# Optimization experiments

Measured on AMD Instinct MI355X. Metric: run time of the kernel, lower is better.

Reference implementation:

```python
import jax, jax.numpy as jnp
import numpy as np

N = 10000       # nodes
E = 640000      # edges (avg degree 64)
F_IN = 128      # num_node_features
H = 128         # hid_size
C = 16          # num_classes


def setup_inputs() -> dict:
    key = jax.random.key(0)
    ks = jax.random.split(key, 12)
    g = lambda k, shape, fan: jax.random.normal(k, shape, jnp.float32) * (1.0 / np.sqrt(fan))
    return {
        "x": jax.random.normal(ks[0], (N, F_IN), jnp.float32),
        "edge_index": jax.random.randint(ks[1], (2, E), 0, N, dtype=jnp.int32),
        "W1": g(ks[2], (F_IN, H), F_IN), "b1": jnp.zeros((H,), jnp.float32),
        "W2": g(ks[3], (H, H), H),       "b2": jnp.zeros((H,), jnp.float32),
        "Wlin1": g(ks[4], (H, C), H),    "blin1": jnp.zeros((C,), jnp.float32),
        "Wdeg2": g(ks[5], (H, 1), H),    "bdeg2": jnp.zeros((1,), jnp.float32),
        "Wdeg3": g(ks[6], (H, 1), H),    "bdeg3": jnp.zeros((1,), jnp.float32),
        "Wdown": g(ks[7], (F_IN, H), F_IN), "bdown": jnp.zeros((H,), jnp.float32),
    }


def _gcn_norm(edge_index):
    # PyG GCNConv: add self-loops, symmetric normalization d^-1/2 A d^-1/2
    loops = jnp.arange(N, dtype=edge_index.dtype)
    src = jnp.concatenate([edge_index[0], loops])   # [E+N]
    dst = jnp.concatenate([edge_index[1], loops])   # [E+N]
    deg = jax.ops.segment_sum(jnp.ones_like(dst, jnp.float32), dst, num_segments=N)
    dis = jnp.where(deg > 0, jax.lax.rsqrt(jnp.maximum(deg, 1.0)), 0.0)
    norm = dis[src] * dis[dst]                      # [E+N]
    return src, dst, norm


def _gcn_conv(h, W, b, src, dst, norm):
    h = h @ W                                       # [N, H] transform first (smaller dim)
    msg = h[src] * norm[:, None]                    # gather + edge weight
    return jax.ops.segment_sum(msg, dst, num_segments=N) + b


def reference(x, edge_index, W1, b1, W2, b2, Wlin1, blin1, Wdeg2, bdeg2, Wdeg3, bdeg3, Wdown, bdown):
    src, dst, norm = _gcn_norm(edge_index)
    original = x @ Wdown + bdown                    # down_sample residual
    h = jax.nn.relu(_gcn_conv(x, W1, b1, src, dst, norm))
    # dropout is identity in eval mode
    h = _gcn_conv(h, W2, b2, src, dst, norm) + original
    result1 = jax.nn.log_softmax(h @ Wlin1 + blin1, axis=1)   # [N, C]
    result2 = (h @ Wdeg2 + bdeg2)[:, 0]                        # [N]
    result3 = (h @ Wdeg3 + bdeg3)[:, 0]                        # [N]
    return (result1, result2, result3)
```

## Files before the change

### kernel.cpp

```cpp
#include <hip/hip_runtime.h>
#include <math.h>

#define N_NODES 10000
#define N_EDGES 640000
#define NB      100
#define CH      (N_EDGES / NB)
#define HP      10016

typedef unsigned short ushort4_t __attribute__((ext_vector_type(4)));
typedef unsigned short ushort8_t __attribute__((ext_vector_type(8)));

__device__ inline unsigned short f2bf(float f) {
    unsigned int u = __float_as_uint(f);
    u = (u + 0x7FFFu + ((u >> 16) & 1u)) >> 16;
    return (unsigned short)u;
}
__device__ inline float bf2f(unsigned short s) {
    return __uint_as_float(((unsigned int)s) << 16);
}

__global__ __launch_bounds__(256) void k_hist(const int* __restrict__ dst,
                                              int* __restrict__ h) {
    __shared__ int hs[HP];
    int t = threadIdx.x;
    for (int j = t; j < HP; j += 256) hs[j] = 0;
    __syncthreads();
    int base = blockIdx.x * CH;
#pragma unroll 4
    for (int j = t; j < CH; j += 256) atomicAdd(&hs[dst[base + j]], 1);
    __syncthreads();
    int* out = h + blockIdx.x * HP;
    for (int j = t; j < N_NODES; j += 256) out[j] = hs[j];
}

__global__ __launch_bounds__(256) void k_colsum(const int* __restrict__ h,
                                                int* __restrict__ deg,
                                                float* __restrict__ dis) {
    int i = blockIdx.x * blockDim.x + threadIdx.x;
    if (i >= N_NODES) return;
    int s = 0;
#pragma unroll 10
    for (int b = 0; b < NB; ++b) s += h[b * HP + i];
    deg[i] = s;
    dis[i] = rsqrtf((float)(s + 1));
}

__global__ void k_scan(const int* __restrict__ deg, int* __restrict__ offsets, int n) {
    __shared__ int sums[1024];
    int tid = threadIdx.x;
    const int per = (n + 1023) / 1024;
    int start = tid * per;
    int end   = min(start + per, n);
    int s = 0;
    for (int i = start; i < end; ++i) s += deg[i];
    sums[tid] = s;
    __syncthreads();
    for (int off = 1; off < 1024; off <<= 1) {
        int t = (tid >= off) ? sums[tid - off] : 0;
        __syncthreads();
        sums[tid] += t;
        __syncthreads();
    }
    int run = sums[tid] - s;
    for (int i = start; i < end; ++i) {
        offsets[i] = run;
        run += deg[i];
    }
    if (tid == 1023) offsets[n] = sums[1023];
}

__global__ __launch_bounds__(256) void k_base(const int* __restrict__ h,
                                              const int* __restrict__ offsets,
                                              int* __restrict__ base) {
    int i = blockIdx.x * blockDim.x + threadIdx.x;
    if (i >= N_NODES) return;
    int run = offsets[i];
#pragma unroll 10
    for (int b = 0; b < NB; ++b) {
        base[b * HP + i] = run;
        run += h[b * HP + i];
    }
}

__global__ __launch_bounds__(256) void k_scatter(const int* __restrict__ src,
                                                 const int* __restrict__ dst,
                                                 const int* __restrict__ base,
                                                 int* __restrict__ csr) {
    __shared__ int cur[N_NODES];
    int t = threadIdx.x;
    const int* mybase = base + blockIdx.x * HP;
    for (int j = t; j < N_NODES; j += 256) cur[j] = mybase[j];
    __syncthreads();
    int off = blockIdx.x * CH;
#pragma unroll 4
    for (int j = t; j < CH; j += 256) {
        int d = dst[off + j];
        int s = src[off + j];
        int p = atomicAdd(&cur[d], 1);
        csr[p] = s;
    }
}

template <int BF16OUT>
__global__ __launch_bounds__(256) void k_gemm(const float* __restrict__ X,
                                              const float* __restrict__ W,
                                              const float* __restrict__ bias,
                                              void* __restrict__ Yv, int n) {
    __shared__ float xs[32 * 128];
    __shared__ float ws[128 * 128];
    int t = threadIdx.x;
    int tile0 = blockIdx.x * 32;

    const float4* Wv = (const float4*)W;
    float4* wsv = (float4*)ws;
#pragma unroll
    for (int q = 0; q < 16; ++q) wsv[t + 256 * q] = Wv[t + 256 * q];

    const float4* Xv = (const float4*)X;
    float4* xsv = (float4*)xs;
#pragma unroll
    for (int q = 0; q < 4; ++q) {
        int idx = t + 256 * q;
        int row = tile0 + (idx >> 5);
        float4 v = make_float4(0.f, 0.f, 0.f, 0.f);
        if (row < n) v = Xv[(size_t)row * 32 + (idx & 31)];
        xsv[idx] = v;
    }
    __syncthreads();

    int c4 = t & 31;
    int rg = t >> 5;
    float4 acc[4];
#pragma unroll
    for (int p = 0; p < 4; ++p) acc[p] = make_float4(0.f, 0.f, 0.f, 0.f);

    const float4* wsr = (const float4*)ws;
    const float4* xsr = (const float4*)xs;
#pragma unroll 4
    for (int kq = 0; kq < 32; ++kq) {
        float4 w0 = wsr[(4 * kq + 0) * 32 + c4];
        float4 w1 = wsr[(4 * kq + 1) * 32 + c4];
        float4 w2 = wsr[(4 * kq + 2) * 32 + c4];
        float4 w3 = wsr[(4 * kq + 3) * 32 + c4];
#pragma unroll
        for (int p = 0; p < 4; ++p) {
            float4 xv = xsr[(rg * 4 + p) * 32 + kq];
            acc[p].x += xv.x * w0.x + xv.y * w1.x + xv.z * w2.x + xv.w * w3.x;
            acc[p].y += xv.x * w0.y + xv.y * w1.y + xv.z * w2.y + xv.w * w3.y;
            acc[p].z += xv.x * w0.z + xv.y * w1.z + xv.z * w2.z + xv.w * w3.z;
            acc[p].w += xv.x * w0.w + xv.y * w1.w + xv.z * w2.w + xv.w * w3.w;
        }
    }
    float4 bv = make_float4(0.f, 0.f, 0.f, 0.f);
    if (bias) bv = ((const float4*)bias)[c4];
#pragma unroll
    for (int p = 0; p < 4; ++p) {
        int row = tile0 + rg * 4 + p;
        if (row < n) {
            float ox = acc[p].x + bv.x, oy = acc[p].y + bv.y;
            float oz = acc[p].z + bv.z, ow = acc[p].w + bv.w;
            if (BF16OUT) {
                ushort4_t o;
                o[0] = f2bf(ox); o[1] = f2bf(oy); o[2] = f2bf(oz); o[3] = f2bf(ow);
                ((ushort4_t*)Yv)[(size_t)row * 32 + c4] = o;
            } else {
                ((float4*)Yv)[(size_t)row * 32 + c4] = make_float4(ox, oy, oz, ow);
            }
        }
    }
}

template <int MODE>
__global__ __launch_bounds__(256) void k_agg(const unsigned short* __restrict__ T,
                                             const float* __restrict__ dis,
                                             const int* __restrict__ offsets,
                                             const int* __restrict__ csr,
                                             const float* __restrict__ bias,
                                             const float* __restrict__ resid,
                                             float* __restrict__ Y, int n) {
    __shared__ float red[3][16][9];
    int i = blockIdx.x;
    int t = threadIdx.x;
    int c8 = t & 15;
    int es = t >> 4;
    int wave = t >> 6;
    int lane = t & 63;

    int e0 = offsets[i], e1 = offsets[i + 1];
    const ushort8_t* T8 = (const ushort8_t*)T;

    float acc[8];
#pragma unroll
    for (int j = 0; j < 8; ++j) acc[j] = 0.f;

    int e = e0 + es;
    for (; e + 16 < e1; e += 32) {
        int s0 = csr[e];
        int s1 = csr[e + 16];
        float w0 = dis[s0];
        float w1 = dis[s1];
        ushort8_t v0 = T8[(size_t)s0 * 16 + c8];
        ushort8_t v1 = T8[(size_t)s1 * 16 + c8];
#pragma unroll
        for (int j = 0; j < 8; ++j)
            acc[j] += w0 * bf2f(v0[j]) + w1 * bf2f(v1[j]);
    }
    if (e < e1) {
        int s0 = csr[e];
        float w0 = dis[s0];
        ushort8_t v0 = T8[(size_t)s0 * 16 + c8];
#pragma unroll
        for (int j = 0; j < 8; ++j) acc[j] += w0 * bf2f(v0[j]);
    }

#pragma unroll
    for (int j = 0; j < 8; ++j) {
        acc[j] += __shfl_xor(acc[j], 16, 64);
        acc[j] += __shfl_xor(acc[j], 32, 64);
    }
    if (wave > 0 && lane < 16) {
#pragma unroll
        for (int j = 0; j < 8; ++j) red[wave - 1][lane][j] = acc[j];
    }
    __syncthreads();
    if (wave == 0 && lane < 16) {
#pragma unroll
        for (int j = 0; j < 8; ++j)
            acc[j] += red[0][lane][j] + red[1][lane][j] + red[2][lane][j];

        float di = dis[i];
        ushort8_t sv = T8[(size_t)i * 16 + c8];
#pragma unroll
        for (int j = 0; j < 8; ++j) acc[j] += di * bf2f(sv[j]);

#pragma unroll
        for (int j = 0; j < 8; ++j) acc[j] = di * acc[j] + bias[c8 * 8 + j];

        if (MODE == 1) {
#pragma unroll
            for (int j = 0; j < 8; ++j) acc[j] = fmaxf(acc[j], 0.f);
        } else {
            const float4* rv4 = (const float4*)resid;
            float4 r0 = rv4[(size_t)i * 32 + c8 * 2];
            float4 r1 = rv4[(size_t)i * 32 + c8 * 2 + 1];
            acc[0] += r0.x; acc[1] += r0.y; acc[2] += r0.z; acc[3] += r0.w;
            acc[4] += r1.x; acc[5] += r1.y; acc[6] += r1.z; acc[7] += r1.w;
        }
        float4* Y4 = (float4*)Y;
        Y4[(size_t)i * 32 + c8 * 2]     = make_float4(acc[0], acc[1], acc[2], acc[3]);
        Y4[(size_t)i * 32 + c8 * 2 + 1] = make_float4(acc[4], acc[5], acc[6], acc[7]);
    }
}

__global__ __launch_bounds__(256) void k_heads(const float* __restrict__ h,
                                               const float* __restrict__ Wlin,
                                               const float* __restrict__ blin,
                                               const float* __restrict__ Wd2,
                                               const float* __restrict__ bd2,
                                               const float* __restrict__ Wd3,
                                               const float* __restrict__ bd3,
                                               float* __restrict__ out1,
                                               float* __restrict__ out2,
                                               float* __restrict__ out3, int n) {
    int wid = (blockIdx.x * blockDim.x + threadIdx.x) >> 6;
    int lane = threadIdx.x & 63;
    if (wid >= n) return;
    int r = wid;
    float h0 = h[(size_t)r * 128 + lane];
    float h1 = h[(size_t)r * 128 + 64 + lane];
    float p2 = h0 * Wd2[lane] + h1 * Wd2[64 + lane];
    float p3 = h0 * Wd3[lane] + h1 * Wd3[64 + lane];
#pragma unroll
    for (int d = 1; d < 64; d <<= 1) {
        p2 += __shfl_xor(p2, d, 64);
        p3 += __shfl_xor(p3, d, 64);
    }
    if (lane == 0) {
        out2[r] = p2 + bd2[0];
        out3[r] = p3 + bd3[0];
    }
    int c = lane & 15, kg = lane >> 4;
    float z = 0.f;
#pragma unroll 8
    for (int j = 0; j < 32; ++j) {
        int k = kg * 32 + j;
        z += h[(size_t)r * 128 + k] * Wlin[k * 16 + c];
    }
    z += __shfl_xor(z, 16, 64);
    z += __shfl_xor(z, 32, 64);
    z += blin[c];
    float m = z;
#pragma unroll
    for (int d = 1; d < 16; d <<= 1) m = fmaxf(m, __shfl_xor(m, d, 64));
    float ex = expf(z - m);
    float ssum = ex;
#pragma unroll
    for (int d = 1; d < 16; d <<= 1) ssum += __shfl_xor(ssum, d, 64);
    float lsm = z - m - logf(ssum);
    if (lane < 16) out1[(size_t)r * 16 + c] = lsm;
}

extern "C" void kernel_launch(void* const* d_in, const int* in_sizes, int n_in,
                              void* d_out, int out_size, void* d_ws, size_t ws_size,
                              hipStream_t stream) {
    const float* x     = (const float*)d_in[0];
    const int*   ei    = (const int*)d_in[1];
    const float* W1    = (const float*)d_in[2];
    const float* b1    = (const float*)d_in[3];
    const float* W2    = (const float*)d_in[4];
    const float* b2    = (const float*)d_in[5];
    const float* Wlin1 = (const float*)d_in[6];
    const float* blin1 = (const float*)d_in[7];
    const float* Wdeg2 = (const float*)d_in[8];
    const float* bdeg2 = (const float*)d_in[9];
    const float* Wdeg3 = (const float*)d_in[10];
    const float* bdeg3 = (const float*)d_in[11];
    const float* Wdown = (const float*)d_in[12];
    const float* bdown = (const float*)d_in[13];

    const int n = N_NODES, E = N_EDGES;
    const int* src = ei;
    const int* dst = ei + E;

    char* ws = (char*)d_ws;
    int*            hmat    = (int*)ws;
    int*            bmat    = hmat + NB * HP;
    int*            deg     = bmat + NB * HP;
    int*            offsets = deg + HP;
    float*          dis     = (float*)(offsets + HP);
    int*            csr     = (int*)(dis + HP);
    unsigned short* bufT    = (unsigned short*)(csr + E);
    float*          bufB    = (float*)(bufT + (size_t)n * 128);
    float*          bufC    = bufB + (size_t)n * 128;

    k_hist<<<NB, 256, 0, stream>>>(dst, hmat);
    k_colsum<<<(n + 255) / 256, 256, 0, stream>>>(hmat, deg, dis);
    k_scan<<<1, 1024, 0, stream>>>(deg, offsets, n);
    k_base<<<(n + 255) / 256, 256, 0, stream>>>(hmat, offsets, bmat);
    k_scatter<<<NB, 256, 0, stream>>>(src, dst, bmat, csr);

    k_gemm<1><<<(n + 31) / 32, 256, 0, stream>>>(x, W1, nullptr, bufT, n);
    k_gemm<0><<<(n + 31) / 32, 256, 0, stream>>>(x, Wdown, bdown, bufB, n);
    k_agg<1><<<n, 256, 0, stream>>>(bufT, dis, offsets, csr, b1, nullptr, bufC, n);
    k_gemm<1><<<(n + 31) / 32, 256, 0, stream>>>(bufC, W2, nullptr, bufT, n);
    k_agg<2><<<n, 256, 0, stream>>>(bufT, dis, offsets, csr, b2, bufB, bufC, n);

    float* out1 = (float*)d_out;
    float* out2 = out1 + (size_t)n * 16;
    float* out3 = out2 + n;
    k_heads<<<(n + 3) / 4, 256, 0, stream>>>(bufC, Wlin1, blin1, Wdeg2, bdeg2,
                                             Wdeg3, bdeg3, out1, out2, out3, n);
}
```

Baseline: 129.2 us.

## Fuse CSR build into one persistent kernel with grid barriers, merge gemms and heads

```diff
diff --git a/kernel.cpp b/kernel.cpp
--- a/kernel.cpp
+++ b/kernel.cpp
@@ -3,8 +3,9 @@
 
 #define N_NODES 10000
 #define N_EDGES 640000
-#define NB      100
-#define CH      (N_EDGES / NB)
+#define NBP     125
+#define CHP     (N_EDGES / NBP)
+#define NPB     (N_NODES / NBP)
 #define HP      10016
 
 typedef unsigned short ushort4_t __attribute__((ext_vector_type(4)));
@@ -19,97 +20,112 @@
     return __uint_as_float(((unsigned int)s) << 16);
 }
 
-__global__ __launch_bounds__(256) void k_hist(const int* __restrict__ dst,
-                                              int* __restrict__ h) {
+__device__ __forceinline__ void gbar(int* bar, int slot) {
+    __syncthreads();
+    if (threadIdx.x == 0) {
+        int* cnt = bar + slot;
+        int* gen = bar + 8 + slot;
+        int g = atomicAdd(gen, 0);
+        __threadfence();
+        if (atomicAdd(cnt, 1) == NBP - 1) {
+            __threadfence();
+            atomicAdd(gen, 1);
+        } else {
+            while (atomicAdd(gen, 0) == g) __builtin_amdgcn_s_sleep(4);
+        }
+        __threadfence();
+    }
+    __syncthreads();
+}
+
+__global__ __launch_bounds__(256) void k_prep(const int* __restrict__ src,
+                                              const int* __restrict__ dst,
+                                              int* bar,
+                                              int* __restrict__ hmat,
+                                              int* __restrict__ bmat,
+                                              int* __restrict__ rangesum,
+                                              int* __restrict__ offsets,
+                                              float* __restrict__ dis,
+                                              int* __restrict__ csr) {
     __shared__ int hs[HP];
-    int t = threadIdx.x;
+    __shared__ int ldeg[NPB];
+    __shared__ int lscan[NPB];
+    __shared__ int rs[NBP];
+    __shared__ int sP;
+    int b = blockIdx.x, t = threadIdx.x;
+
     for (int j = t; j < HP; j += 256) hs[j] = 0;
     __syncthreads();
-    int base = blockIdx.x * CH;
+    const int* mydst = dst + b * CHP;
 #pragma unroll 4
-    for (int j = t; j < CH; j += 256) atomicAdd(&hs[dst[base + j]], 1);
-    __syncthreads();
-    int* out = h + blockIdx.x * HP;
-    for (int j = t; j < N_NODES; j += 256) out[j] = hs[j];
-}
-
-__global__ __launch_bounds__(256) void k_colsum(const int* __restrict__ h,
-                                                int* __restrict__ deg,
-                                                float* __restrict__ dis) {
-    int i = blockIdx.x * blockDim.x + threadIdx.x;
-    if (i >= N_NODES) return;
-    int s = 0;
-#pragma unroll 10
-    for (int b = 0; b < NB; ++b) s += h[b * HP + i];
-    deg[i] = s;
-    dis[i] = rsqrtf((float)(s + 1));
-}
-
-__global__ void k_scan(const int* __restrict__ deg, int* __restrict__ offsets, int n) {
-    __shared__ int sums[1024];
-    int tid = threadIdx.x;
-    const int per = (n + 1023) / 1024;
-    int start = tid * per;
-    int end   = min(start + per, n);
-    int s = 0;
-    for (int i = start; i < end; ++i) s += deg[i];
-    sums[tid] = s;
-    __syncthreads();
-    for (int off = 1; off < 1024; off <<= 1) {
-        int t = (tid >= off) ? sums[tid - off] : 0;
-        __syncthreads();
-        sums[tid] += t;
-        __syncthreads();
-    }
-    int run = sums[tid] - s;
-    for (int i = start; i < end; ++i) {
+    for (int j = t; j < CHP; j += 256) atomicAdd(&hs[mydst[j]], 1);
+    __syncthreads();
+    int* hrow = hmat + b * HP;
+    for (int j = t; j < N_NODES; j += 256) hrow[j] = hs[j];
+    gbar(bar, 0);
+
+    int i0 = b * NPB;
+    if (t < NPB) {
+        int i = i0 + t;
+        int s = 0;
+#pragma unroll 5
+        for (int bb = 0; bb < NBP; ++bb) s += hmat[bb * HP + i];
+        ldeg[t] = s;
+        dis[i] = rsqrtf((float)(s + 1));
+    }
+    __syncthreads();
+    if (t == 0) {
+        int s = 0;
+        for (int j = 0; j < NPB; ++j) { lscan[j] = s; s += ldeg[j]; }
+        rangesum[b] = s;
+    }
+    gbar(bar, 1);
+
+    if (t < NBP) rs[t] = rangesum[t];
+    __syncthreads();
+    if (t == 0) {
+        int P = 0;
+        for (int bb = 0; bb < b; ++bb) P += rs[bb];
+        sP = P;
+        if (b == NBP - 1) offsets[N_NODES] = P + rs[b];
+    }
+    __syncthreads();
+    if (t < NPB) {
+        int i = i0 + t;
+        int run = sP + lscan[t];
         offsets[i] = run;
-        run += deg[i];
-    }
-    if (tid == 1023) offsets[n] = sums[1023];
-}
-
-__global__ __launch_bounds__(256) void k_base(const int* __restrict__ h,
-                                              const int* __restrict__ offsets,
-                                              int* __restrict__ base) {
-    int i = blockIdx.x * blockDim.x + threadIdx.x;
-    if (i >= N_NODES) return;
-    int run = offsets[i];
-#pragma unroll 10
-    for (int b = 0; b < NB; ++b) {
-        base[b * HP + i] = run;
-        run += h[b * HP + i];
-    }
-}
-
-__global__ __launch_bounds__(256) void k_scatter(const int* __restrict__ src,
-                                                 const int* __restrict__ dst,
-                                                 const int* __restrict__ base,
-                                                 int* __restrict__ csr) {
-    __shared__ int cur[N_NODES];
-    int t = threadIdx.x;
-    const int* mybase = base + blockIdx.x * HP;
-    for (int j = t; j < N_NODES; j += 256) cur[j] = mybase[j];
-    __syncthreads();
-    int off = blockIdx.x * CH;
+#pragma unroll 5
+        for (int bb = 0; bb < NBP; ++bb) {
+            bmat[bb * HP + i] = run;
+            run += hmat[bb * HP + i];
+        }
+    }
+    gbar(bar, 2);
+
+    const int* myb = bmat + b * HP;
+    for (int j = t; j < N_NODES; j += 256) hs[j] = myb[j];
+    __syncthreads();
+    const int* mysrc = src + b * CHP;
 #pragma unroll 4
-    for (int j = t; j < CH; j += 256) {
-        int d = dst[off + j];
-        int s = src[off + j];
-        int p = atomicAdd(&cur[d], 1);
+    for (int j = t; j < CHP; j += 256) {
+        int d = mydst[j];
+        int s = mysrc[j];
+        int p = atomicAdd(&hs[d], 1);
         csr[p] = s;
     }
 }
 
-template <int BF16OUT>
-__global__ __launch_bounds__(256) void k_gemm(const float* __restrict__ X,
-                                              const float* __restrict__ W,
-                                              const float* __restrict__ bias,
-                                              void* __restrict__ Yv, int n) {
+__global__ __launch_bounds__(256) void k_gemm2(const float* __restrict__ X,
+                                               const float* __restrict__ W1,
+                                               const float* __restrict__ Wdown,
+                                               const float* __restrict__ bdown,
+                                               unsigned short* __restrict__ outT,
+                                               float* __restrict__ outB, int n) {
     __shared__ float xs[32 * 128];
     __shared__ float ws[128 * 128];
     int t = threadIdx.x;
     int tile0 = blockIdx.x * 32;
+    const float* W = blockIdx.y ? Wdown : W1;
 
     const float4* Wv = (const float4*)W;
     float4* wsv = (float4*)ws;
@@ -151,33 +167,98 @@
             acc[p].w += xv.x * w0.w + xv.y * w1.w + xv.z * w2.w + xv.w * w3.w;
         }
     }
-    float4 bv = make_float4(0.f, 0.f, 0.f, 0.f);
-    if (bias) bv = ((const float4*)bias)[c4];
+    if (blockIdx.y == 0) {
+#pragma unroll
+        for (int p = 0; p < 4; ++p) {
+            int row = tile0 + rg * 4 + p;
+            if (row < n) {
+                ushort4_t o;
+                o[0] = f2bf(acc[p].x); o[1] = f2bf(acc[p].y);
+                o[2] = f2bf(acc[p].z); o[3] = f2bf(acc[p].w);
+                ((ushort4_t*)outT)[(size_t)row * 32 + c4] = o;
+            }
+        }
+    } else {
+        float4 bv = ((const float4*)bdown)[c4];
+#pragma unroll
+        for (int p = 0; p < 4; ++p) {
+            int row = tile0 + rg * 4 + p;
+            if (row < n) {
+                float4 o;
+                o.x = acc[p].x + bv.x; o.y = acc[p].y + bv.y;
+                o.z = acc[p].z + bv.z; o.w = acc[p].w + bv.w;
+                ((float4*)outB)[(size_t)row * 32 + c4] = o;
+            }
+        }
+    }
+}
+
+__global__ __launch_bounds__(256) void k_gemm(const float* __restrict__ X,
+                                              const float* __restrict__ W,
+                                              unsigned short* __restrict__ Y, int n) {
+    __shared__ float xs[32 * 128];
+    __shared__ float ws[128 * 128];
+    int t = threadIdx.x;
+    int tile0 = blockIdx.x * 32;
+
+    const float4* Wv = (const float4*)W;
+    float4* wsv = (float4*)ws;
+#pragma unroll
+    for (int q = 0; q < 16; ++q) wsv[t + 256 * q] = Wv[t + 256 * q];
+
+    const float4* Xv = (const float4*)X;
+    float4* xsv = (float4*)xs;
+#pragma unroll
+    for (int q = 0; q < 4; ++q) {
+        int idx = t + 256 * q;
+        int row = tile0 + (idx >> 5);
+        float4 v = make_float4(0.f, 0.f, 0.f, 0.f);
+        if (row < n) v = Xv[(size_t)row * 32 + (idx & 31)];
+        xsv[idx] = v;
+    }
+    __syncthreads();
+
+    int c4 = t & 31;
+    int rg = t >> 5;
+    float4 acc[4];
+#pragma unroll
+    for (int p = 0; p < 4; ++p) acc[p] = make_float4(0.f, 0.f, 0.f, 0.f);
+
+    const float4* wsr = (const float4*)ws;
+    const float4* xsr = (const float4*)xs;
+#pragma unroll 4
+    for (int kq = 0; kq < 32; ++kq) {
+        float4 w0 = wsr[(4 * kq + 0) * 32 + c4];
+        float4 w1 = wsr[(4 * kq + 1) * 32 + c4];
+        float4 w2 = wsr[(4 * kq + 2) * 32 + c4];
+        float4 w3 = wsr[(4 * kq + 3) * 32 + c4];
+#pragma unroll
+        for (int p = 0; p < 4; ++p) {
+            float4 xv = xsr[(rg * 4 + p) * 32 + kq];
+            acc[p].x += xv.x * w0.x + xv.y * w1.x + xv.z * w2.x + xv.w * w3.x;
+            acc[p].y += xv.x * w0.y + xv.y * w1.y + xv.z * w2.y + xv.w * w3.y;
+            acc[p].z += xv.x * w0.z + xv.y * w1.z + xv.z * w2.z + xv.w * w3.z;
+            acc[p].w += xv.x * w0.w + xv.y * w1.w + xv.z * w2.w + xv.w * w3.w;
+        }
+    }
 #pragma unroll
     for (int p = 0; p < 4; ++p) {
         int row = tile0 + rg * 4 + p;
         if (row < n) {
-            float ox = acc[p].x + bv.x, oy = acc[p].y + bv.y;
-            float oz = acc[p].z + bv.z, ow = acc[p].w + bv.w;
-            if (BF16OUT) {
-                ushort4_t o;
-                o[0] = f2bf(ox); o[1] = f2bf(oy); o[2] = f2bf(oz); o[3] = f2bf(ow);
-                ((ushort4_t*)Yv)[(size_t)row * 32 + c4] = o;
-            } else {
-                ((float4*)Yv)[(size_t)row * 32 + c4] = make_float4(ox, oy, oz, ow);
-            }
-        }
-    }
-}
-
-template <int MODE>
-__global__ __launch_bounds__(256) void k_agg(const unsigned short* __restrict__ T,
-                                             const float* __restrict__ dis,
-                                             const int* __restrict__ offsets,
-                                             const int* __restrict__ csr,
-                                             const float* __restrict__ bias,
-                                             const float* __restrict__ resid,
-                                             float* __restrict__ Y, int n) {
+            ushort4_t o;
+            o[0] = f2bf(acc[p].x); o[1] = f2bf(acc[p].y);
+            o[2] = f2bf(acc[p].z); o[3] = f2bf(acc[p].w);
+            ((ushort4_t*)Y)[(size_t)row * 32 + c4] = o;
+        }
+    }
+}
+
+__global__ __launch_bounds__(256) void k_agg1(const unsigned short* __restrict__ T,
+                                              const float* __restrict__ dis,
+                                              const int* __restrict__ offsets,
+                                              const int* __restrict__ csr,
+                                              const float* __restrict__ bias,
+                                              float* __restrict__ Y, int n) {
     __shared__ float red[3][16][9];
     int i = blockIdx.x;
     int t = threadIdx.x;
@@ -232,27 +313,22 @@
         ushort8_t sv = T8[(size_t)i * 16 + c8];
 #pragma unroll
         for (int j = 0; j < 8; ++j) acc[j] += di * bf2f(sv[j]);
-
-#pragma unroll
-        for (int j = 0; j < 8; ++j) acc[j] = di * acc[j] + bias[c8 * 8 + j];
-
-        if (MODE == 1) {
-#pragma unroll
-            for (int j = 0; j < 8; ++j) acc[j] = fmaxf(acc[j], 0.f);
-        } else {
-            const float4* rv4 = (const float4*)resid;
-            float4 r0 = rv4[(size_t)i * 32 + c8 * 2];
-            float4 r1 = rv4[(size_t)i * 32 + c8 * 2 + 1];
-            acc[0] += r0.x; acc[1] += r0.y; acc[2] += r0.z; acc[3] += r0.w;
-            acc[4] += r1.x; acc[5] += r1.y; acc[6] += r1.z; acc[7] += r1.w;
-        }
+#pragma unroll
+        for (int j = 0; j < 8; ++j)
+            acc[j] = fmaxf(di * acc[j] + bias[c8 * 8 + j], 0.f);
+
         float4* Y4 = (float4*)Y;
         Y4[(size_t)i * 32 + c8 * 2]     = make_float4(acc[0], acc[1], acc[2], acc[3]);
         Y4[(size_t)i * 32 + c8 * 2 + 1] = make_float4(acc[4], acc[5], acc[6], acc[7]);
     }
 }
 
-__global__ __launch_bounds__(256) void k_heads(const float* __restrict__ h,
+__global__ __launch_bounds__(256) void k_agg2h(const unsigned short* __restrict__ T,
+                                               const float* __restrict__ dis,
+                                               const int* __restrict__ offsets,
+                                               const int* __restrict__ csr,
+                                               const float* __restrict__ bias,
+                                               const float* __restrict__ resid,
                                                const float* __restrict__ Wlin,
                                                const float* __restrict__ blin,
                                                const float* __restrict__ Wd2,
@@ -262,42 +338,109 @@
                                                float* __restrict__ out1,
                                                float* __restrict__ out2,
                                                float* __restrict__ out3, int n) {
-    int wid = (blockIdx.x * blockDim.x + threadIdx.x) >> 6;
-    int lane = threadIdx.x & 63;
-    if (wid >= n) return;
-    int r = wid;
-    float h0 = h[(size_t)r * 128 + lane];
-    float h1 = h[(size_t)r * 128 + 64 + lane];
-    float p2 = h0 * Wd2[lane] + h1 * Wd2[64 + lane];
-    float p3 = h0 * Wd3[lane] + h1 * Wd3[64 + lane];
-#pragma unroll
-    for (int d = 1; d < 64; d <<= 1) {
-        p2 += __shfl_xor(p2, d, 64);
-        p3 += __shfl_xor(p3, d, 64);
-    }
-    if (lane == 0) {
-        out2[r] = p2 + bd2[0];
-        out3[r] = p3 + bd3[0];
-    }
-    int c = lane & 15, kg = lane >> 4;
-    float z = 0.f;
+    __shared__ float red[3][16][9];
+    __shared__ float hrow[128];
+    int i = blockIdx.x;
+    int t = threadIdx.x;
+    int c8 = t & 15;
+    int es = t >> 4;
+    int wave = t >> 6;
+    int lane = t & 63;
+
+    int e0 = offsets[i], e1 = offsets[i + 1];
+    const ushort8_t* T8 = (const ushort8_t*)T;
+
+    float acc[8];
+#pragma unroll
+    for (int j = 0; j < 8; ++j) acc[j] = 0.f;
+
+    int e = e0 + es;
+    for (; e + 16 < e1; e += 32) {
+        int s0 = csr[e];
+        int s1 = csr[e + 16];
+        float w0 = dis[s0];
+        float w1 = dis[s1];
+        ushort8_t v0 = T8[(size_t)s0 * 16 + c8];
+        ushort8_t v1 = T8[(size_t)s1 * 16 + c8];
+#pragma unroll
+        for (int j = 0; j < 8; ++j)
+            acc[j] += w0 * bf2f(v0[j]) + w1 * bf2f(v1[j]);
+    }
+    if (e < e1) {
+        int s0 = csr[e];
+        float w0 = dis[s0];
+        ushort8_t v0 = T8[(size_t)s0 * 16 + c8];
+#pragma unroll
+        for (int j = 0; j < 8; ++j) acc[j] += w0 * bf2f(v0[j]);
+    }
+
+#pragma unroll
+    for (int j = 0; j < 8; ++j) {
+        acc[j] += __shfl_xor(acc[j], 16, 64);
+        acc[j] += __shfl_xor(acc[j], 32, 64);
+    }
+    if (wave > 0 && lane < 16) {
+#pragma unroll
+        for (int j = 0; j < 8; ++j) red[wave - 1][lane][j] = acc[j];
+    }
+    __syncthreads();
+    if (wave == 0 && lane < 16) {
+#pragma unroll
+        for (int j = 0; j < 8; ++j)
+            acc[j] += red[0][lane][j] + red[1][lane][j] + red[2][lane][j];
+
+        float di = dis[i];
+        ushort8_t sv = T8[(size_t)i * 16 + c8];
+#pragma unroll
+        for (int j = 0; j < 8; ++j) acc[j] += di * bf2f(sv[j]);
+
+        const float4* rv4 = (const float4*)resid;
+        float4 r0 = rv4[(size_t)i * 32 + c8 * 2];
+        float4 r1 = rv4[(size_t)i * 32 + c8 * 2 + 1];
+#pragma unroll
+        for (int j = 0; j < 8; ++j) acc[j] = di * acc[j] + bias[c8 * 8 + j];
+        acc[0] += r0.x; acc[1] += r0.y; acc[2] += r0.z; acc[3] += r0.w;
+        acc[4] += r1.x; acc[5] += r1.y; acc[6] += r1.z; acc[7] += r1.w;
+
+#pragma unroll
+        for (int j = 0; j < 8; ++j) hrow[c8 * 8 + j] = acc[j];
+    }
+    __syncthreads();
+
+    if (wave == 0) {
+        float h0 = hrow[lane];
+        float h1 = hrow[64 + lane];
+        float p2 = h0 * Wd2[lane] + h1 * Wd2[64 + lane];
+        float p3 = h0 * Wd3[lane] + h1 * Wd3[64 + lane];
+#pragma unroll
+        for (int d = 1; d < 64; d <<= 1) {
+            p2 += __shfl_xor(p2, d, 64);
+            p3 += __shfl_xor(p3, d, 64);
+        }
+        if (lane == 0) {
+            out2[i] = p2 + bd2[0];
+            out3[i] = p3 + bd3[0];
+        }
+        int c = lane & 15, kg = lane >> 4;
+        float z = 0.f;
 #pragma unroll 8
-    for (int j = 0; j < 32; ++j) {
-        int k = kg * 32 + j;
-        z += h[(size_t)r * 128 + k] * Wlin[k * 16 + c];
-    }
-    z += __shfl_xor(z, 16, 64);
-    z += __shfl_xor(z, 32, 64);
-    z += blin[c];
-    float m = z;
-#pragma unroll
-    for (int d = 1; d < 16; d <<= 1) m = fmaxf(m, __shfl_xor(m, d, 64));
-    float ex = expf(z - m);
-    float ssum = ex;
-#pragma unroll
-    for (int d = 1; d < 16; d <<= 1) ssum += __shfl_xor(ssum, d, 64);
-    float lsm = z - m - logf(ssum);
-    if (lane < 16) out1[(size_t)r * 16 + c] = lsm;
+        for (int j = 0; j < 32; ++j) {
+            int k = kg * 32 + j;
+            z += hrow[k] * Wlin[k * 16 + c];
+        }
+        z += __shfl_xor(z, 16, 64);
+        z += __shfl_xor(z, 32, 64);
+        z += blin[c];
+        float m = z;
+#pragma unroll
+        for (int d = 1; d < 16; d <<= 1) m = fmaxf(m, __shfl_xor(m, d, 64));
+        float ex = expf(z - m);
+        float ssum = ex;
+#pragma unroll
+        for (int d = 1; d < 16; d <<= 1) ssum += __shfl_xor(ssum, d, 64);
+        float lsm = z - m - logf(ssum);
+        if (lane < 16) out1[(size_t)i * 16 + c] = lsm;
+    }
 }
 
 extern "C" void kernel_launch(void* const* d_in, const int* in_sizes, int n_in,
@@ -323,31 +466,30 @@
     const int* dst = ei + E;
 
     char* ws = (char*)d_ws;
-    int*            hmat    = (int*)ws;
-    int*            bmat    = hmat + NB * HP;
-    int*            deg     = bmat + NB * HP;
-    int*            offsets = deg + HP;
-    float*          dis     = (float*)(offsets + HP);
-    int*            csr     = (int*)(dis + HP);
-    unsigned short* bufT    = (unsigned short*)(csr + E);
-    float*          bufB    = (float*)(bufT + (size_t)n * 128);
-    float*          bufC    = bufB + (size_t)n * 128;
-
-    k_hist<<<NB, 256, 0, stream>>>(dst, hmat);
-    k_colsum<<<(n + 255) / 256, 256, 0, stream>>>(hmat, deg, dis);
-    k_scan<<<1, 1024, 0, stream>>>(deg, offsets, n);
-    k_base<<<(n + 255) / 256, 256, 0, stream>>>(hmat, offsets, bmat);
-    k_scatter<<<NB, 256, 0, stream>>>(src, dst, bmat, csr);
-
-    k_gemm<1><<<(n + 31) / 32, 256, 0, stream>>>(x, W1, nullptr, bufT, n);
-    k_gemm<0><<<(n + 31) / 32, 256, 0, stream>>>(x, Wdown, bdown, bufB, n);
-    k_agg<1><<<n, 256, 0, stream>>>(bufT, dis, offsets, csr, b1, nullptr, bufC, n);
-    k_gemm<1><<<(n + 31) / 32, 256, 0, stream>>>(bufC, W2, nullptr, bufT, n);
-    k_agg<2><<<n, 256, 0, stream>>>(bufT, dis, offsets, csr, b2, bufB, bufC, n);
+    int*            bar      = (int*)ws;
+    int*            hmat     = bar + 64;
+    int*            bmat     = hmat + NBP * HP;
+    int*            rangesum = bmat + NBP * HP;
+    int*            offsets  = rangesum + 128;
+    float*          dis      = (float*)(offsets + 10048);
+    int*            csr      = (int*)(dis + HP);
+    unsigned short* bufT     = (unsigned short*)(csr + E);
+    float*          bufB     = (float*)(bufT + (size_t)n * 128);
+    float*          bufC     = bufB + (size_t)n * 128;
+
+    hipMemsetAsync(bar, 0, 64 * sizeof(int), stream);
+
+    k_prep<<<NBP, 256, 0, stream>>>(src, dst, bar, hmat, bmat, rangesum,
+                                    offsets, dis, csr);
+    k_gemm2<<<dim3((n + 31) / 32, 2), 256, 0, stream>>>(x, W1, Wdown, bdown,
+                                                        bufT, bufB, n);
+    k_agg1<<<n, 256, 0, stream>>>(bufT, dis, offsets, csr, b1, bufC, n);
+    k_gemm<<<(n + 31) / 32, 256, 0, stream>>>(bufC, W2, bufT, n);
 
     float* out1 = (float*)d_out;
     float* out2 = out1 + (size_t)n * 16;
     float* out3 = out2 + n;
-    k_heads<<<(n + 3) / 4, 256, 0, stream>>>(bufC, Wlin1, blin1, Wdeg2, bdeg2,
-                                             Wdeg3, bdeg3, out1, out2, out3, n);
-}
+    k_agg2h<<<n, 256, 0, stream>>>(bufT, dis, offsets, csr, b2, bufB,
+                                   Wlin1, blin1, Wdeg2, bdeg2, Wdeg3, bdeg3,
+                                   out1, out2, out3, n);
+}
```

Result: slower. 151.1 us (+16.9%).
